# Kernel tuning notes

Measured on AMD Instinct MI355X. Metric: run time of the kernel, lower is better.

The kernel has to match this reference:

```python
import jax, jax.numpy as jnp
import numpy as np

ALPHA = 0.9
COLUMNS = (0,)
PRE_STEP = 0


def setup_inputs() -> dict:
    key = jax.random.key(0)
    x = jax.random.normal(key, (32, 4096, 256), dtype=jnp.float32)
    return {"x": x}


def _ema(x):
    # out[:, 0] = x[:, 0]; out[:, i] = alpha * out[:, i-1] + (1 - alpha) * x[:, i]
    # Linear recurrence y_i = a_i * y_{i-1} + b_i solved with a log-depth
    # associative scan: combine((a1,b1),(a2,b2)) = (a1*a2, a2*b1 + b2).
    B, T, C = x.shape
    a = jnp.full((1, T, 1), ALPHA, dtype=x.dtype).at[:, 0, :].set(0.0)
    b = jnp.concatenate([x[:, :1, :], (1.0 - ALPHA) * x[:, 1:, :]], axis=1)

    def combine(left, right):
        a_l, b_l = left
        a_r, b_r = right
        return (a_l * a_r, a_r * b_l + b_r)

    _, out = jax.lax.associative_scan(combine, (a, b), axis=1)
    return out


def reference(x):
    out = _ema(x)
    T = out.shape[1]
    tail = out[:, T - 1 - PRE_STEP:T, :][:, :, jnp.asarray(COLUMNS)]  # [B, pre_step+1, len(columns)]
    return (out, tail)
```

## Files before the change

### kernel.cpp

```cpp
#include <hip/hip_runtime.h>


#define B_   32
#define T_   4096
#define C_   256
#define CG   64
#define L_   256
#define W_   32
#define NC   16
#define PF   8
#define BLK  64

#define ALPHA 0.9f
#define OMA   0.1f

typedef float f32x4 __attribute__((ext_vector_type(4)));

__device__ __forceinline__ f32x4 ema_step(f32x4 y, f32x4 v) {
    f32x4 r;
    r.x = fmaf(ALPHA, y.x, OMA * v.x);
    r.y = fmaf(ALPHA, y.y, OMA * v.y);
    r.z = fmaf(ALPHA, y.z, OMA * v.z);
    r.w = fmaf(ALPHA, y.w, OMA * v.w);
    return r;
}

template<int TOT, int WARM>
__device__ __forceinline__ f32x4 scan_run(const f32x4* __restrict__ xb,
                                          f32x4* __restrict__ op, f32x4 y) {
    constexpr int NB = TOT / PF;
    static_assert(TOT % PF == 0 && NB % 2 == 0, "batch geometry");
    f32x4 bufA[PF], bufB[PF];
    #pragma unroll
    for (int i = 0; i < PF; ++i) bufA[i] = xb[(size_t)i * CG];
    #pragma unroll
    for (int i = 0; i < PF; ++i) bufB[i] = xb[(size_t)(PF + i) * CG];

    #pragma unroll
    for (int p = 0; p < NB / 2; ++p) {
        const int kA = 2 * p, kB = 2 * p + 1;
        #pragma unroll
        for (int i = 0; i < PF; ++i) {
            y = ema_step(y, bufA[i]);
            const int t = kA * PF + i;
            if (t >= WARM)
                op[(size_t)(t - WARM) * CG] = y;
        }
        if (kA + 2 < NB) {
            #pragma unroll
            for (int i = 0; i < PF; ++i)
                bufA[i] = xb[(size_t)((kA + 2) * PF + i) * CG];
        }
        #pragma unroll
        for (int i = 0; i < PF; ++i) {
            y = ema_step(y, bufB[i]);
            const int t = kB * PF + i;
            if (t >= WARM)
                op[(size_t)(t - WARM) * CG] = y;
        }
        if (kB + 2 < NB) {
            #pragma unroll
            for (int i = 0; i < PF; ++i)
                bufB[i] = xb[(size_t)((kB + 2) * PF + i) * CG];
        }
    }
    return y;
}

__global__ __launch_bounds__(BLK) void ema_fused(const float* __restrict__ x,
                                                 float* __restrict__ out,
                                                 float* __restrict__ tail) {
    int bid = (int)blockIdx.x;
    int swz = (bid & 7) * ((int)gridDim.x >> 3) + (bid >> 3);
    int tid = swz * BLK + (int)threadIdx.x;

    int cg    = tid & (CG - 1);
    int bc    = tid >> 6;
    int chunk = bc & (NC - 1);
    int b     = bc >> 4;
    int start = chunk * L_;

    const f32x4* xs = reinterpret_cast<const f32x4*>(x)
                    + ((size_t)(b * T_ + start)) * CG + cg;
    f32x4* op = reinterpret_cast<f32x4*>(out)
              + ((size_t)(b * T_ + start)) * CG + cg;

    f32x4 y;
    if (chunk == 0) {
        y = xs[0];
        y = scan_run<L_, 0>(xs, op, y);
    } else {
        y = scan_run<L_ + W_, W_>(xs - (size_t)W_ * CG, op, (f32x4)(0.f));
    }
    if (chunk == NC - 1 && cg == 0) {
        tail[b] = y.x;
    }
}

extern "C" void kernel_launch(void* const* d_in, const int* in_sizes, int n_in,
                              void* d_out, int out_size, void* d_ws, size_t ws_size,
                              hipStream_t stream) {
    const float* x = (const float*)d_in[0];
    float* out  = (float*)d_out;
    float* tail = out + (size_t)B_ * T_ * C_;

    int threads = B_ * NC * CG;
    ema_fused<<<threads / BLK, BLK, 0, stream>>>(x, out, tail);
}
```

Before: 45.15 us.

## Switch to float2 per-thread columns with longer time chunks

Each thread now owns two channels (float2) instead of four, so there are 128 column groups per batch. Time is split into 8 chunks of 512 steps rather than 16 of 256, and each prefetch batch is 16 steps instead of 8. Thread count stays the same, and the warm-up recomputation overhead drops from 32/256 to 32/512 per chunk. In exchange, memory accesses become 8-byte instead of 16-byte and each thread runs a serial recurrence twice as long, which lowers memory-level parallelism per instruction.

```diff
diff --git a/kernel.cpp b/kernel.cpp
--- a/kernel.cpp
+++ b/kernel.cpp
@@ -4,37 +4,35 @@
 #define B_   32
 #define T_   4096
 #define C_   256
-#define CG   64
-#define L_   256
+#define CG2  128
+#define L_   512
 #define W_   32
-#define NC   16
-#define PF   8
+#define NC   8
+#define PF   16
 #define BLK  64
 
 #define ALPHA 0.9f
 #define OMA   0.1f
 
-typedef float f32x4 __attribute__((ext_vector_type(4)));
+typedef float f32x2 __attribute__((ext_vector_type(2)));
 
-__device__ __forceinline__ f32x4 ema_step(f32x4 y, f32x4 v) {
-    f32x4 r;
+__device__ __forceinline__ f32x2 ema_step(f32x2 y, f32x2 v) {
+    f32x2 r;
     r.x = fmaf(ALPHA, y.x, OMA * v.x);
     r.y = fmaf(ALPHA, y.y, OMA * v.y);
-    r.z = fmaf(ALPHA, y.z, OMA * v.z);
-    r.w = fmaf(ALPHA, y.w, OMA * v.w);
     return r;
 }
 
 template<int TOT, int WARM>
-__device__ __forceinline__ f32x4 scan_run(const f32x4* __restrict__ xb,
-                                          f32x4* __restrict__ op, f32x4 y) {
+__device__ __forceinline__ f32x2 scan_run(const f32x2* __restrict__ xb,
+                                          f32x2* __restrict__ op, f32x2 y) {
     constexpr int NB = TOT / PF;
     static_assert(TOT % PF == 0 && NB % 2 == 0, "batch geometry");
-    f32x4 bufA[PF], bufB[PF];
+    f32x2 bufA[PF], bufB[PF];
     #pragma unroll
-    for (int i = 0; i < PF; ++i) bufA[i] = xb[(size_t)i * CG];
+    for (int i = 0; i < PF; ++i) bufA[i] = xb[(size_t)i * CG2];
     #pragma unroll
-    for (int i = 0; i < PF; ++i) bufB[i] = xb[(size_t)(PF + i) * CG];
+    for (int i = 0; i < PF; ++i) bufB[i] = xb[(size_t)(PF + i) * CG2];
 
     #pragma unroll
     for (int p = 0; p < NB / 2; ++p) {
@@ -44,24 +42,24 @@
             y = ema_step(y, bufA[i]);
             const int t = kA * PF + i;
             if (t >= WARM)
-                op[(size_t)(t - WARM) * CG] = y;
+                op[(size_t)(t - WARM) * CG2] = y;
         }
         if (kA + 2 < NB) {
             #pragma unroll
             for (int i = 0; i < PF; ++i)
-                bufA[i] = xb[(size_t)((kA + 2) * PF + i) * CG];
+                bufA[i] = xb[(size_t)((kA + 2) * PF + i) * CG2];
         }
         #pragma unroll
         for (int i = 0; i < PF; ++i) {
             y = ema_step(y, bufB[i]);
             const int t = kB * PF + i;
             if (t >= WARM)
-                op[(size_t)(t - WARM) * CG] = y;
+                op[(size_t)(t - WARM) * CG2] = y;
         }
         if (kB + 2 < NB) {
             #pragma unroll
             for (int i = 0; i < PF; ++i)
-                bufB[i] = xb[(size_t)((kB + 2) * PF + i) * CG];
+                bufB[i] = xb[(size_t)((kB + 2) * PF + i) * CG2];
         }
     }
     return y;
@@ -74,23 +72,23 @@
     int swz = (bid & 7) * ((int)gridDim.x >> 3) + (bid >> 3);
     int tid = swz * BLK + (int)threadIdx.x;
 
-    int cg    = tid & (CG - 1);
-    int bc    = tid >> 6;
+    int cg    = tid & (CG2 - 1);
+    int bc    = tid >> 7;
     int chunk = bc & (NC - 1);
-    int b     = bc >> 4;
+    int b     = bc >> 3;
     int start = chunk * L_;
 
-    const f32x4* xs = reinterpret_cast<const f32x4*>(x)
-                    + ((size_t)(b * T_ + start)) * CG + cg;
-    f32x4* op = reinterpret_cast<f32x4*>(out)
-              + ((size_t)(b * T_ + start)) * CG + cg;
+    const f32x2* xs = reinterpret_cast<const f32x2*>(x)
+                    + ((size_t)(b * T_ + start)) * CG2 + cg;
+    f32x2* op = reinterpret_cast<f32x2*>(out)
+              + ((size_t)(b * T_ + start)) * CG2 + cg;
 
-    f32x4 y;
+    f32x2 y;
     if (chunk == 0) {
         y = xs[0];
         y = scan_run<L_, 0>(xs, op, y);
     } else {
-        y = scan_run<L_ + W_, W_>(xs - (size_t)W_ * CG, op, (f32x4)(0.f));
+        y = scan_run<L_ + W_, W_>(xs - (size_t)W_ * CG2, op, (f32x2)(0.f));
     }
     if (chunk == NC - 1 && cg == 0) {
         tail[b] = y.x;
@@ -104,6 +102,6 @@
     float* out  = (float*)d_out;
     float* tail = out + (size_t)B_ * T_ * C_;
 
-    int threads = B_ * NC * CG;
+    int threads = B_ * NC * CG2;
     ema_fused<<<threads / BLK, BLK, 0, stream>>>(x, out, tail);
 }
```

Result: faster. 44.15 us (-2.2%).
